# Performance work log

Hardware: AMD Instinct MI355X
Metric: run time of the kernel (lower is better)

The kernel has to match this reference:

```python
import jax, jax.numpy as jnp
import numpy as np


def setup_inputs() -> dict:
    key = jax.random.key(0)
    ks = jax.random.split(key, 6)
    B, S, H, O, E = 4, 2048, 4096, 4096, 4
    x = jax.random.normal(ks[0], (B, S, H), dtype=jnp.float32)
    weight = jax.random.normal(ks[1], (O, H), dtype=jnp.float32)
    bias = jax.random.normal(ks[2], (O,), dtype=jnp.float32)
    gate_w = jax.random.normal(ks[3], (E, H), dtype=jnp.float32) * 0.02
    in_channel_scale = jax.random.normal(ks[4], (E, H), dtype=jnp.float32)
    out_channel_scale = jax.random.normal(ks[5], (E, O), dtype=jnp.float32)
    return {"x": x, "weight": weight, "bias": bias, "gate_w": gate_w,
            "in_channel_scale": in_channel_scale, "out_channel_scale": out_channel_scale}


def reference(x, weight, bias, gate_w, in_channel_scale, out_channel_scale):
    *lead, H = x.shape
    O = weight.shape[0]
    xf = x.reshape(-1, H)                                   # [N, H]
    # gating: Linear(H, E, bias=False) -> softmax in fp32, cast back
    router_logits = xf @ gate_w.T                           # [N, E]
    routing_weights = jax.nn.softmax(router_logits.astype(jnp.float32), axis=1).astype(x.dtype)
    in_scale = routing_weights @ in_channel_scale           # [N, H]
    out_scale = routing_weights @ out_channel_scale         # [N, O]
    bin_w = jnp.sign(weight)                                # STE sign forward
    y = ((xf * in_scale) @ bin_w.T) * out_scale + bias      # [N, O]
    return y.reshape(*lead, O)
```

## Files before the change

### kernel.cpp

```cpp
#include <hip/hip_runtime.h>
#include <hip/hip_bf16.h>

#define H_DIM 4096
#define O_DIM 4096
#define N_ROWS 8192

typedef __bf16 bf16x8 __attribute__((ext_vector_type(8)));
typedef float  f32x4  __attribute__((ext_vector_type(4)));

__device__ __forceinline__ unsigned short f32_bf16_rne(float f) {
    unsigned int u = __builtin_bit_cast(unsigned int, f);
    u += 0x7FFFu + ((u >> 16) & 1u);
    return (unsigned short)(u >> 16);
}

__device__ __forceinline__ void gload_lds16(const unsigned short* g, unsigned short* l) {
    __builtin_amdgcn_global_load_lds((const __attribute__((address_space(1))) void*)g,
                                     (__attribute__((address_space(3))) void*)l,
                                     16, 0, 0);
}

__global__ void __launch_bounds__(256) sign_kernel(const float* __restrict__ w,
                                                   unsigned short* __restrict__ bw) {
    size_t i = ((size_t)blockIdx.x * 256 + threadIdx.x) * 4;
    float4 v = *reinterpret_cast<const float4*>(w + i);
    ushort4 o;
    o.x = v.x > 0.f ? 0x3F80 : (v.x < 0.f ? 0xBF80 : 0);
    o.y = v.y > 0.f ? 0x3F80 : (v.y < 0.f ? 0xBF80 : 0);
    o.z = v.z > 0.f ? 0x3F80 : (v.z < 0.f ? 0xBF80 : 0);
    o.w = v.w > 0.f ? 0x3F80 : (v.w < 0.f ? 0xBF80 : 0);
    *reinterpret_cast<ushort4*>(bw + i) = o;
}

__global__ void __launch_bounds__(256) route_scale_kernel(
    const float* __restrict__ x, const float* __restrict__ gate_w,
    const float* __restrict__ ics, float* __restrict__ rw_out,
    unsigned short* __restrict__ xs_out)
{
    __shared__ float red[4][4];
    const int n = blockIdx.x;
    const int t = threadIdx.x;
    const float* xr = x + (size_t)n * H_DIM;

    float4 xv[4];
    float lg[4] = {0.f, 0.f, 0.f, 0.f};
#pragma unroll
    for (int c = 0; c < 4; ++c) {
        const int idx = c * 1024 + t * 4;
        xv[c] = *reinterpret_cast<const float4*>(xr + idx);
#pragma unroll
        for (int e = 0; e < 4; ++e) {
            float4 g = *reinterpret_cast<const float4*>(gate_w + e * H_DIM + idx);
            lg[e] += xv[c].x * g.x + xv[c].y * g.y + xv[c].z * g.z + xv[c].w * g.w;
        }
    }
#pragma unroll
    for (int e = 0; e < 4; ++e) {
#pragma unroll
        for (int off = 1; off < 64; off <<= 1)
            lg[e] += __shfl_xor(lg[e], off, 64);
    }
    if ((t & 63) == 0) {
        const int w = t >> 6;
        red[w][0] = lg[0]; red[w][1] = lg[1]; red[w][2] = lg[2]; red[w][3] = lg[3];
    }
    __syncthreads();
    const float l0 = red[0][0] + red[1][0] + red[2][0] + red[3][0];
    const float l1 = red[0][1] + red[1][1] + red[2][1] + red[3][1];
    const float l2 = red[0][2] + red[1][2] + red[2][2] + red[3][2];
    const float l3 = red[0][3] + red[1][3] + red[2][3] + red[3][3];
    const float m  = fmaxf(fmaxf(l0, l1), fmaxf(l2, l3));
    const float p0 = expf(l0 - m), p1 = expf(l1 - m), p2 = expf(l2 - m), p3 = expf(l3 - m);
    const float inv = 1.f / (p0 + p1 + p2 + p3);
    const float w0 = p0 * inv, w1 = p1 * inv, w2 = p2 * inv, w3 = p3 * inv;
    if (t == 0) {
        float4 wv = make_float4(w0, w1, w2, w3);
        *reinterpret_cast<float4*>(rw_out + (size_t)n * 4) = wv;
    }
#pragma unroll
    for (int c = 0; c < 4; ++c) {
        const int idx = c * 1024 + t * 4;
        float4 i0 = *reinterpret_cast<const float4*>(ics + 0 * H_DIM + idx);
        float4 i1 = *reinterpret_cast<const float4*>(ics + 1 * H_DIM + idx);
        float4 i2 = *reinterpret_cast<const float4*>(ics + 2 * H_DIM + idx);
        float4 i3 = *reinterpret_cast<const float4*>(ics + 3 * H_DIM + idx);
        const float sx = w0 * i0.x + w1 * i1.x + w2 * i2.x + w3 * i3.x;
        const float sy = w0 * i0.y + w1 * i1.y + w2 * i2.y + w3 * i3.y;
        const float sz = w0 * i0.z + w1 * i1.z + w2 * i2.z + w3 * i3.z;
        const float sw = w0 * i0.w + w1 * i1.w + w2 * i2.w + w3 * i3.w;
        ushort4 o;
        o.x = f32_bf16_rne(xv[c].x * sx);
        o.y = f32_bf16_rne(xv[c].y * sy);
        o.z = f32_bf16_rne(xv[c].z * sz);
        o.w = f32_bf16_rne(xv[c].w * sw);
        *reinterpret_cast<ushort4*>(xs_out + (size_t)n * H_DIM + idx) = o;
    }
}


#define GATE4 asm volatile("s_waitcnt vmcnt(4)" ::: "memory")
#define GATE0 asm volatile("s_waitcnt vmcnt(0)" ::: "memory")
#define NOGATE

#define WINDOW(W, CA_, CB_, NA_, NB_, DO_STAGE, GATE_STMT, DO_READS, DO_BAR)    \
  {                                                                             \
    const int w_ = (W);                                                         \
    if (DO_STAGE) {                                                             \
      const int ks_ = w_ + 3;                                                   \
      char* sA_ = lds + (ks_ & 3) * 16384;                                      \
      char* sB_ = lds + 65536 + (ks_ & 3) * 16384;                              \
      _Pragma("unroll")                                                         \
      for (int j = 0; j < 2; ++j) {                                             \
        gload_lds16(gA + ((size_t)j * 128) * H_DIM + ks_ * 32,                  \
                    (unsigned short*)(sA_ + j * 8192 + wv * 1024));             \
        gload_lds16(gB + ((size_t)j * 128) * H_DIM + ks_ * 32,                  \
                    (unsigned short*)(sB_ + j * 8192 + wv * 1024));             \
      }                                                                         \
    }                                                                           \
    GATE_STMT;                                                                  \
    if (DO_READS) {                                                             \
      const int sb_ = ((w_ + 1) & 3) * 16384;                                   \
      _Pragma("unroll")                                                         \
      for (int fr = 0; fr < 8; ++fr)                                            \
        NA_[fr] = *reinterpret_cast<const bf16x8*>(lds + sb_ + aOff[fr]);       \
      _Pragma("unroll")                                                         \
      for (int ni = 0; ni < 4; ++ni)                                            \
        NB_[ni] = *reinterpret_cast<const bf16x8*>(lds + 65536 + sb_ + bOff[ni]); \
    }                                                                           \
    __builtin_amdgcn_s_setprio(1);                                              \
    _Pragma("unroll")                                                           \
    for (int fr = 0; fr < 8; ++fr)                                              \
      _Pragma("unroll")                                                         \
      for (int ni = 0; ni < 4; ++ni)                                            \
        acc[fr][ni] = __builtin_amdgcn_mfma_f32_16x16x32_bf16(CA_[fr], CB_[ni], \
                                                              acc[fr][ni], 0, 0, 0); \
    __builtin_amdgcn_s_setprio(0);                                              \
    if (DO_BAR) __builtin_amdgcn_s_barrier();                                   \
  }

__global__ void __launch_bounds__(512, 2) gemm_bin_kernel(
    const unsigned short* __restrict__ xs,
    const unsigned short* __restrict__ bw,
    const float* __restrict__ rw,
    const float* __restrict__ ocs,
    const float* __restrict__ bias,
    float* __restrict__ out)
{
    __shared__ __align__(16) char lds[131072];

    const int t  = threadIdx.x;
    const int wv = t >> 6;
    const int ln = t & 63;
    const int wr = wv >> 2;
    const int wc = wv & 3;

    const int bid = blockIdx.x;
    const int swz = (bid & 7) * 64 + (bid >> 3);
    const int rowBase = (swz >> 4) * 256;
    const int colBase = (swz & 15) * 256;

    const int s_r  = t >> 2;
    const int s_cl = (t & 3) ^ ((t >> 3) & 3);
    const unsigned short* gA = xs + (size_t)(rowBase + s_r) * H_DIM + s_cl * 8;
    const unsigned short* gB = bw + (size_t)(colBase + s_r) * H_DIM + s_cl * 8;

    int aOff[8], bOff[4];
#pragma unroll
    for (int fr = 0; fr < 8; ++fr) {
        const int row = wr * 128 + fr * 16 + (ln & 15);
        aOff[fr] = row * 64 + (((ln >> 4) ^ ((row >> 1) & 3)) << 4);
    }
#pragma unroll
    for (int ni = 0; ni < 4; ++ni) {
        const int row = wc * 64 + ni * 16 + (ln & 15);
        bOff[ni] = row * 64 + (((ln >> 4) ^ ((row >> 1) & 3)) << 4);
    }

    f32x4 acc[8][4];
#pragma unroll
    for (int i = 0; i < 8; ++i)
#pragma unroll
        for (int j = 0; j < 4; ++j) acc[i][j] = (f32x4){0.f, 0.f, 0.f, 0.f};

#pragma unroll
    for (int kt = 0; kt < 3; ++kt) {
        char* sA = lds + kt * 16384;
        char* sB = lds + 65536 + kt * 16384;
#pragma unroll
        for (int j = 0; j < 2; ++j) {
            gload_lds16(gA + ((size_t)j * 128) * H_DIM + kt * 32,
                        (unsigned short*)(sA + j * 8192 + wv * 1024));
            gload_lds16(gB + ((size_t)j * 128) * H_DIM + kt * 32,
                        (unsigned short*)(sB + j * 8192 + wv * 1024));
        }
    }
    GATE4;
    __builtin_amdgcn_s_barrier();

    bf16x8 avA[8], bvA[4], avB[8], bvB[4];
#pragma unroll
    for (int fr = 0; fr < 8; ++fr)
        avA[fr] = *reinterpret_cast<const bf16x8*>(lds + aOff[fr]);
#pragma unroll
    for (int ni = 0; ni < 4; ++ni)
        bvA[ni] = *reinterpret_cast<const bf16x8*>(lds + 65536 + bOff[ni]);

    for (int w = 0; w < 124; w += 2) {
        WINDOW(w,     avA, bvA, avB, bvB, 1, GATE4, 1, 1);
        WINDOW(w + 1, avB, bvB, avA, bvA, 1, GATE4, 1, 1);
    }
    WINDOW(124, avA, bvA, avB, bvB, 1, GATE4,  1, 1);
    WINDOW(125, avB, bvB, avA, bvA, 0, GATE0,  1, 1);
    WINDOW(126, avA, bvA, avB, bvB, 0, NOGATE, 1, 1);
    WINDOW(127, avB, bvB, avA, bvA, 0, NOGATE, 0, 0);

    float oce[4][4], bve[4];
    int cole[4];
#pragma unroll
    for (int ni = 0; ni < 4; ++ni) {
        const int col = colBase + wc * 64 + ni * 16 + (ln & 15);
        cole[ni] = col;
        oce[ni][0] = ocs[0 * O_DIM + col];
        oce[ni][1] = ocs[1 * O_DIM + col];
        oce[ni][2] = ocs[2 * O_DIM + col];
        oce[ni][3] = ocs[3 * O_DIM + col];
        bve[ni] = bias[col];
    }
#pragma unroll
    for (int fr = 0; fr < 8; ++fr) {
        float4 rwv[4];
        int rowe[4];
#pragma unroll
        for (int j = 0; j < 4; ++j) {
            const int row = rowBase + wr * 128 + fr * 16 + (ln >> 4) * 4 + j;
            rowe[j] = row;
            rwv[j] = *reinterpret_cast<const float4*>(rw + (size_t)row * 4);
        }
#pragma unroll
        for (int ni = 0; ni < 4; ++ni) {
#pragma unroll
            for (int j = 0; j < 4; ++j) {
                const float os = rwv[j].x * oce[ni][0] + rwv[j].y * oce[ni][1] +
                                 rwv[j].z * oce[ni][2] + rwv[j].w * oce[ni][3];
                out[(size_t)rowe[j] * O_DIM + cole[ni]] = acc[fr][ni][j] * os + bve[ni];
            }
        }
    }
}

extern "C" void kernel_launch(void* const* d_in, const int* in_sizes, int n_in,
                              void* d_out, int out_size, void* d_ws, size_t ws_size,
                              hipStream_t stream) {
    const float* x      = (const float*)d_in[0];
    const float* weight = (const float*)d_in[1];
    const float* bias   = (const float*)d_in[2];
    const float* gate_w = (const float*)d_in[3];
    const float* ics    = (const float*)d_in[4];
    const float* ocs    = (const float*)d_in[5];
    float* out = (float*)d_out;

    unsigned short* xs = (unsigned short*)d_ws;
    unsigned short* bw = xs + (size_t)N_ROWS * H_DIM;
    float* rw = (float*)(bw + (size_t)O_DIM * H_DIM);

    sign_kernel<<<(O_DIM * H_DIM) / (256 * 4), 256, 0, stream>>>(weight, bw);
    route_scale_kernel<<<N_ROWS, 256, 0, stream>>>(x, gate_w, ics, rw, xs);
    gemm_bin_kernel<<<(N_ROWS / 256) * (O_DIM / 256), 512, 0, stream>>>(xs, bw, rw, ocs, bias, out);
}
```

Baseline: 317.9 us.

## Load B fragments directly from global into registers, bypassing LDS

The binarized weight (B) tiles are no longer staged through LDS. Each wave now loads its own B fragments straight from global memory into registers one window ahead, while A keeps the LDS pipeline. This halves LDS usage to 64KB, which could allow two blocks per CU, and removes the B LDS reads and writes. In exchange, each wave pair with the same column issues duplicate strided global loads, and that global latency is hidden behind only one window of MFMAs. The vmcnt gates are adjusted and moved to after the MFMA block to account for the extra outstanding loads.

```diff
diff --git a/kernel.cpp b/kernel.cpp
--- a/kernel.cpp
+++ b/kernel.cpp
@@ -98,34 +98,32 @@
 }
 
 
+#define GATE6 asm volatile("s_waitcnt vmcnt(6)" ::: "memory")
 #define GATE4 asm volatile("s_waitcnt vmcnt(4)" ::: "memory")
 #define GATE0 asm volatile("s_waitcnt vmcnt(0)" ::: "memory")
 #define NOGATE
 
-#define WINDOW(W, CA_, CB_, NA_, NB_, DO_STAGE, GATE_STMT, DO_READS, DO_BAR)    \
+#define WINDOW(W, CA_, CB_, NA_, NB_, DO_STAGE, GATE_STMT, DO_B, DO_READS, DO_BAR) \
   {                                                                             \
     const int w_ = (W);                                                         \
     if (DO_STAGE) {                                                             \
       const int ks_ = w_ + 3;                                                   \
       char* sA_ = lds + (ks_ & 3) * 16384;                                      \
-      char* sB_ = lds + 65536 + (ks_ & 3) * 16384;                              \
-      _Pragma("unroll")                                                         \
-      for (int j = 0; j < 2; ++j) {                                             \
+      _Pragma("unroll")                                                         \
+      for (int j = 0; j < 2; ++j)                                               \
         gload_lds16(gA + ((size_t)j * 128) * H_DIM + ks_ * 32,                  \
                     (unsigned short*)(sA_ + j * 8192 + wv * 1024));             \
-        gload_lds16(gB + ((size_t)j * 128) * H_DIM + ks_ * 32,                  \
-                    (unsigned short*)(sB_ + j * 8192 + wv * 1024));             \
-      }                                                                         \
     }                                                                           \
-    GATE_STMT;                                                                  \
+    if (DO_B) {                                                                 \
+      _Pragma("unroll")                                                         \
+      for (int ni = 0; ni < 4; ++ni)                                            \
+        NB_[ni] = *reinterpret_cast<const bf16x8*>(gBr[ni] + (size_t)(w_ + 1) * 32); \
+    }                                                                           \
     if (DO_READS) {                                                             \
       const int sb_ = ((w_ + 1) & 3) * 16384;                                   \
       _Pragma("unroll")                                                         \
       for (int fr = 0; fr < 8; ++fr)                                            \
         NA_[fr] = *reinterpret_cast<const bf16x8*>(lds + sb_ + aOff[fr]);       \
-      _Pragma("unroll")                                                         \
-      for (int ni = 0; ni < 4; ++ni)                                            \
-        NB_[ni] = *reinterpret_cast<const bf16x8*>(lds + 65536 + sb_ + bOff[ni]); \
     }                                                                           \
     __builtin_amdgcn_s_setprio(1);                                              \
     _Pragma("unroll")                                                           \
@@ -135,6 +133,7 @@
         acc[fr][ni] = __builtin_amdgcn_mfma_f32_16x16x32_bf16(CA_[fr], CB_[ni], \
                                                               acc[fr][ni], 0, 0, 0); \
     __builtin_amdgcn_s_setprio(0);                                              \
+    GATE_STMT;                                                                  \
     if (DO_BAR) __builtin_amdgcn_s_barrier();                                   \
   }
 
@@ -146,7 +145,7 @@
     const float* __restrict__ bias,
     float* __restrict__ out)
 {
-    __shared__ __align__(16) char lds[131072];
+    __shared__ __align__(16) char lds[65536];
 
     const int t  = threadIdx.x;
     const int wv = t >> 6;
@@ -162,57 +161,54 @@
     const int s_r  = t >> 2;
     const int s_cl = (t & 3) ^ ((t >> 3) & 3);
     const unsigned short* gA = xs + (size_t)(rowBase + s_r) * H_DIM + s_cl * 8;
-    const unsigned short* gB = bw + (size_t)(colBase + s_r) * H_DIM + s_cl * 8;
-
-    int aOff[8], bOff[4];
+
+    const unsigned short* gBr[4];
+#pragma unroll
+    for (int ni = 0; ni < 4; ++ni)
+        gBr[ni] = bw + (size_t)(colBase + wc * 64 + ni * 16 + (ln & 15)) * H_DIM
+                     + (ln >> 4) * 8;
+
+    int aOff[8];
 #pragma unroll
     for (int fr = 0; fr < 8; ++fr) {
         const int row = wr * 128 + fr * 16 + (ln & 15);
         aOff[fr] = row * 64 + (((ln >> 4) ^ ((row >> 1) & 3)) << 4);
     }
-#pragma unroll
-    for (int ni = 0; ni < 4; ++ni) {
-        const int row = wc * 64 + ni * 16 + (ln & 15);
-        bOff[ni] = row * 64 + (((ln >> 4) ^ ((row >> 1) & 3)) << 4);
-    }
 
     f32x4 acc[8][4];
 #pragma unroll
     for (int i = 0; i < 8; ++i)
 #pragma unroll
         for (int j = 0; j < 4; ++j) acc[i][j] = (f32x4){0.f, 0.f, 0.f, 0.f};
+
+    bf16x8 avA[8], bvA[4], avB[8], bvB[4];
 
 #pragma unroll
     for (int kt = 0; kt < 3; ++kt) {
         char* sA = lds + kt * 16384;
-        char* sB = lds + 65536 + kt * 16384;
-#pragma unroll
-        for (int j = 0; j < 2; ++j) {
+#pragma unroll
+        for (int j = 0; j < 2; ++j)
             gload_lds16(gA + ((size_t)j * 128) * H_DIM + kt * 32,
                         (unsigned short*)(sA + j * 8192 + wv * 1024));
-            gload_lds16(gB + ((size_t)j * 128) * H_DIM + kt * 32,
-                        (unsigned short*)(sB + j * 8192 + wv * 1024));
-        }
-    }
-    GATE4;
+    }
+#pragma unroll
+    for (int ni = 0; ni < 4; ++ni)
+        bvA[ni] = *reinterpret_cast<const bf16x8*>(gBr[ni]);
+    GATE6;
     __builtin_amdgcn_s_barrier();
 
-    bf16x8 avA[8], bvA[4], avB[8], bvB[4];
 #pragma unroll
     for (int fr = 0; fr < 8; ++fr)
         avA[fr] = *reinterpret_cast<const bf16x8*>(lds + aOff[fr]);
-#pragma unroll
-    for (int ni = 0; ni < 4; ++ni)
-        bvA[ni] = *reinterpret_cast<const bf16x8*>(lds + 65536 + bOff[ni]);
 
     for (int w = 0; w < 124; w += 2) {
-        WINDOW(w,     avA, bvA, avB, bvB, 1, GATE4, 1, 1);
-        WINDOW(w + 1, avB, bvB, avA, bvA, 1, GATE4, 1, 1);
-    }
-    WINDOW(124, avA, bvA, avB, bvB, 1, GATE4,  1, 1);
-    WINDOW(125, avB, bvB, avA, bvA, 0, GATE0,  1, 1);
-    WINDOW(126, avA, bvA, avB, bvB, 0, NOGATE, 1, 1);
-    WINDOW(127, avB, bvB, avA, bvA, 0, NOGATE, 0, 0);
+        WINDOW(w,     avA, bvA, avB, bvB, 1, GATE6, 1, 1, 1);
+        WINDOW(w + 1, avB, bvB, avA, bvA, 1, GATE6, 1, 1, 1);
+    }
+    WINDOW(124, avA, bvA, avB, bvB, 1, GATE6,  1, 1, 1);
+    WINDOW(125, avB, bvB, avA, bvA, 0, GATE4,  1, 1, 1);
+    WINDOW(126, avA, bvA, avB, bvB, 0, GATE0,  1, 1, 1);
+    WINDOW(127, avB, bvB, avA, bvA, 0, NOGATE, 0, 0, 0);
 
     float oce[4][4], bve[4];
     int cole[4];
```

Result: slower. 452.0 us (+42.2%).
